# Optimization experiments

Hardware: AMD Instinct MI355X
Metric: run time of the kernel (lower is better)

The kernel has to match this reference:

```python
import jax, jax.numpy as jnp
import numpy as np

B, S, T, D, H, DF = 2, 2048, 2048, 1024, 16, 4096
DK = D // H
EPS = 1e-5


def _linear_params(key, d_in, d_out):
    kw, kb = jax.random.split(key)
    s = 1.0 / np.sqrt(d_in)
    W = jax.random.uniform(kw, (d_out, d_in), jnp.float32, -s, s)
    b = jax.random.uniform(kb, (d_out,), jnp.float32, -s, s)
    return W, b


def setup_inputs() -> dict:
    key = jax.random.key(0)
    ks = jax.random.split(key, 16)
    inp = {}
    inp['x'] = jax.random.normal(ks[0], (B, S, D), jnp.float32)
    inp['enc_out'] = jax.random.normal(ks[1], (B, T, D), jnp.float32)
    inp['src_mask'] = jnp.ones((B, 1, 1, T), jnp.int32)
    inp['tgt_mask'] = jnp.tril(jnp.ones((S, S), jnp.int32))[None, None, :, :]
    # self-attn params
    for i, nm in enumerate(['q1', 'k1', 'v1', 'o1']):
        W, b = _linear_params(ks[2 + i], D, D)
        inp['W' + nm], inp['b' + nm] = W, b
    # cross-attn params
    for i, nm in enumerate(['q2', 'k2', 'v2', 'o2']):
        W, b = _linear_params(ks[6 + i], D, D)
        inp['W' + nm], inp['b' + nm] = W, b
    # FFN
    inp['Wf1'], inp['bf1'] = _linear_params(ks[10], D, DF)
    inp['Wf2'], inp['bf2'] = _linear_params(ks[11], DF, D)
    # LayerNorms
    for i in (1, 2, 3):
        inp[f'g{i}'] = jnp.ones((D,), jnp.float32)
        inp[f'be{i}'] = jnp.zeros((D,), jnp.float32)
    return inp


def _lin(x, W, b):
    return x @ W.T + b


def _ln(x, g, b):
    mu = jnp.mean(x, -1, keepdims=True)
    var = jnp.mean(jnp.square(x - mu), -1, keepdims=True)
    return (x - mu) * jax.lax.rsqrt(var + EPS) * g + b


def _mha(q_in, k_in, v_in, Wq, bq, Wk, bk, Wv, bv, Wo, bo, mask):
    Bq = q_in.shape[0]
    q = _lin(q_in, Wq, bq).reshape(Bq, -1, H, DK).transpose(0, 2, 1, 3)
    k = _lin(k_in, Wk, bk).reshape(Bq, -1, H, DK).transpose(0, 2, 1, 3)
    v = _lin(v_in, Wv, bv).reshape(Bq, -1, H, DK).transpose(0, 2, 1, 3)
    scores = jnp.einsum('bhqd,bhkd->bhqk', q, k) / np.sqrt(DK)
    scores = jnp.where(mask == 0, -jnp.inf, scores)
    attn = jax.nn.softmax(scores, axis=-1)
    out = jnp.einsum('bhqk,bhkd->bhqd', attn, v)
    out = out.transpose(0, 2, 1, 3).reshape(Bq, -1, H * DK)
    return _lin(out, Wo, bo)


def reference(x, enc_out, src_mask, tgt_mask,
              Wq1, bq1, Wk1, bk1, Wv1, bv1, Wo1, bo1,
              Wq2, bq2, Wk2, bk2, Wv2, bv2, Wo2, bo2,
              Wf1, bf1, Wf2, bf2,
              g1, be1, g2, be2, g3, be3):
    out = _mha(x, x, x, Wq1, bq1, Wk1, bk1, Wv1, bv1, Wo1, bo1, tgt_mask)
    x = _ln(x + out, g1, be1)
    out = _mha(x, enc_out, enc_out, Wq2, bq2, Wk2, bk2, Wv2, bv2, Wo2, bo2, src_mask)
    x = _ln(x + out, g2, be2)
    ff = _lin(jax.nn.relu(_lin(x, Wf1, bf1)), Wf2, bf2)
    return _ln(x + ff, g3, be3)
```

## Files before the change

kernel.cpp:

```cpp
#include <hip/hip_runtime.h>


typedef __bf16 bf16_t;
typedef bf16_t  bf16x8 __attribute__((ext_vector_type(8)));
typedef float   f32x4  __attribute__((ext_vector_type(4)));
typedef unsigned short ushort_t;
typedef ushort_t u16x8 __attribute__((ext_vector_type(8)));
typedef ushort_t u16x4 __attribute__((ext_vector_type(4)));

__device__ __forceinline__ float b2f(ushort_t u) {
    union { unsigned u; float f; } x; x.u = ((unsigned)u) << 16; return x.f;
}
__device__ __forceinline__ ushort_t f2b(float f) {
    union { float f; unsigned u; } x; x.f = f;
    unsigned r = x.u + 0x7fffu + ((x.u >> 16) & 1u);
    return (ushort_t)(r >> 16);
}
__device__ __forceinline__ unsigned pk2(float lo, float hi) {
    union { float f; unsigned u; } a, b; a.f = lo; b.f = hi;
    return (b.u & 0xffff0000u) | (a.u >> 16);
}

#define GLL(gp, lp)                                                            \
    __builtin_amdgcn_global_load_lds(                                          \
        (const __attribute__((address_space(1))) void*)(gp),                   \
        (__attribute__((address_space(3))) void*)(lp), 16, 0, 0)

__global__ __launch_bounds__(256) void conv_all(
    const float* __restrict__ x,   const float* __restrict__ enc,
    const float* __restrict__ w0, const float* __restrict__ w1,
    const float* __restrict__ w2, const float* __restrict__ w3,
    const float* __restrict__ w4, const float* __restrict__ w5,
    const float* __restrict__ w6, const float* __restrict__ w7,
    const float* __restrict__ wf1, const float* __restrict__ wf2,
    ushort_t* __restrict__ Xb, ushort_t* __restrict__ Eb,
    ushort_t* __restrict__ Wb)
{
    const int b = blockIdx.x;
    const float* src;
    ushort_t* dst;
    size_t blk;
    if (b < 2048)      { src = x;   dst = Xb; blk = b; }
    else if (b < 4096) { src = enc; dst = Eb; blk = b - 2048; }
    else if (b < 8192) {
        const int i = (b - 4096) >> 9;
        src = (i < 4) ? (i < 2 ? (i == 0 ? w0 : w1) : (i == 2 ? w2 : w3))
                      : (i < 6 ? (i == 4 ? w4 : w5) : (i == 6 ? w6 : w7));
        dst = Wb + (size_t)i * 1048576;
        blk = (b - 4096) & 511;
    }
    else if (b < 10240) { src = wf1; dst = Wb + (size_t)8  * 1048576; blk = b - 8192; }
    else                { src = wf2; dst = Wb + (size_t)12 * 1048576; blk = b - 10240; }

    const size_t e = blk * 2048 + (size_t)threadIdx.x * 8;
    const float4 a = *(const float4*)(src + e);
    const float4 c = *(const float4*)(src + e + 4);
    uint4 r;
    r.x = pk2(a.x, a.y); r.y = pk2(a.z, a.w);
    r.z = pk2(c.x, c.y); r.w = pk2(c.z, c.w);
    *(uint4*)(dst + e) = r;
}

template <int EPI, int TM, bool RF32, bool FUSED, bool SPLITA, bool SPLITC,
          bool TRV>
__global__ __launch_bounds__(256) void gemm_bt(
    const ushort_t* __restrict__ A, const ushort_t* __restrict__ A2,
    const ushort_t* __restrict__ W,
    const float* __restrict__ b1, const float* __restrict__ b2,
    const float* __restrict__ b3,
    const void* __restrict__ Rv,
    ushort_t* __restrict__ C, ushort_t* __restrict__ C2,
    int M, int N, int K)
{
    constexpr int IM = TM / 32;
    __shared__ __align__(16) ushort_t At[TM * 32];
    __shared__ __align__(16) ushort_t Bt[128 * 32];

    const int tid  = threadIdx.x;
    const int lane = tid & 63, w = tid >> 6;
    const int g = lane >> 4, qi = lane & 15;

    const int nbn = gridDim.x, nbm = gridDim.y;
    const int lin = blockIdx.x + nbn * blockIdx.y;
    const int xcd = lin & 7, j = lin >> 3;
    const int bpx = nbm >> 3;
    const int bmb = xcd * bpx + (j & (bpx - 1));
    const int bnb = j / bpx;
    const int bm = bmb * TM, bn = bnb * 128;

    const int wm = (w >> 1) * (TM / 2), wn = (w & 1) * 64;

    const ushort_t* Ap = SPLITA ? ((bm < 2048) ? A : A2) : A;
    const int       am = SPLITA ? (bm & 2047) : bm;

    const int srow = lane >> 2;
    const int scol = (lane & 3) * 8;

    f32x4 acc[IM][4] = {};

    const int niter = K >> 5;
    for (int kt = 0; kt < niter; ++kt) {
        const int k0 = kt << 5;
        __syncthreads();
        if (TM == 128) {
#pragma unroll
            for (int c = 0; c < 2; ++c) {
                const int s = c * 4 + w;
                GLL(Ap + (size_t)(am + s * 16 + srow) * K + k0 + scol, At + s * 512);
            }
        } else {
            GLL(Ap + (size_t)(am + w * 16 + srow) * K + k0 + scol, At + w * 512);
        }
#pragma unroll
        for (int c = 0; c < 2; ++c) {
            const int s = c * 4 + w;
            GLL(W + (size_t)(bn + s * 16 + srow) * K + k0 + scol, Bt + s * 512);
        }
        __syncthreads();

        bf16x8 af[IM], bfr[4];
#pragma unroll
        for (int i = 0; i < IM; ++i)
            af[i] = *(const bf16x8*)(At + (wm + i * 16 + qi) * 32 + g * 8);
#pragma unroll
        for (int j2 = 0; j2 < 4; ++j2)
            bfr[j2] = *(const bf16x8*)(Bt + (wn + j2 * 16 + qi) * 32 + g * 8);
#pragma unroll
        for (int i = 0; i < IM; ++i)
#pragma unroll
            for (int j2 = 0; j2 < 4; ++j2)
                acc[i][j2] = __builtin_amdgcn_mfma_f32_16x16x32_bf16(
                    af[i], bfr[j2], acc[i][j2], 0, 0, 0);
    }

    const float* bp = FUSED ? (bn < 1024 ? b1 : (bn < 2048 ? b2 : b3)) : b1;
#pragma unroll
    for (int j2 = 0; j2 < 4; ++j2) {
        const int n = bn + wn + j2 * 16 + qi;
        const int nl = n & 1023;
        const float bv = bp[nl];
#pragma unroll
        for (int i = 0; i < IM; ++i) {
            if (EPI == 1 && TRV && bn >= N - 1024) {
                const int which = bn >> 10;
                const int h = nl >> 6, dk = nl & 63;
                const int m0 = bm + wm + i * 16 + g * 4;
                const int bb = m0 >> 11, s0 = m0 & 2047;
                u16x4 pv;
#pragma unroll
                for (int r = 0; r < 4; ++r) pv[r] = f2b(acc[i][j2][r] + bv);
                *(u16x4*)(C + (size_t)which * 4194304 +
                          (((size_t)((bb << 4) + h)) * 64 + dk) * 2048 + s0) = pv;
            } else {
#pragma unroll
                for (int r = 0; r < 4; ++r) {
                    const int m = bm + wm + i * 16 + g * 4 + r;
                    float v = acc[i][j2][r] + bv;
                    if (EPI == 2) {
                        v += RF32 ? ((const float*)Rv)[(size_t)m * N + n]
                                  : b2f(((const ushort_t*)Rv)[(size_t)m * N + n]);
                    }
                    if (EPI == 3) v = v > 0.f ? v : 0.f;
                    if (EPI == 1) {
                        const int which = FUSED ? (bn >> 10) : 0;
                        const int bb = m >> 11, s = m & 2047;
                        const int h = nl >> 6, dk = nl & 63;
                        const size_t dst = (size_t)which * 4194304 +
                            (((size_t)((bb << 4) + h)) * 2048 + s) * 64 + dk;
                        C[dst] = f2b(v);
                    } else {
                        ushort_t* Cp = SPLITC ? (m < 2048 ? C : C2) : C;
                        const int mr = SPLITC ? (m & 2047) : m;
                        Cp[(size_t)mr * N + n] = f2b(v);
                    }
                }
            }
        }
    }
}

template <bool CAUSAL>
__global__ __launch_bounds__(256) void flash_attn(
    const ushort_t* __restrict__ Q, const ushort_t* __restrict__ K,
    const ushort_t* __restrict__ V, ushort_t* __restrict__ O, int S)
{
    __shared__ __align__(16) ushort_t Kt[2][2048];
    __shared__ __align__(16) ushort_t Vt[2][2048];
    __shared__ __align__(16) ushort_t Pl[2048];

    const int tid = threadIdx.x, lane = tid & 63, w = tid >> 6;
    const int g = lane >> 4, qi = lane & 15;
    const int q2 = (qi >> 1) & 3;
    const int bh = blockIdx.x;
    const int y = blockIdx.y;
    const int qb = CAUSAL ? ((y & 8) ? ((y & 16) ? 55 - y : 23 - y) : y) : y;
    const size_t base = (size_t)bh * S * 64;
    const int q0 = qb << 6;
    const int qw = q0 + w * 16;

    constexpr float SC = 0.18033688011112042f;

    const int krow2 = ((w & 1) << 4) + (lane >> 2);
    const int kcol2 = ((w >> 1) << 5) + ((lane & 3) << 3);
    const ushort_t* Kp = K + base + (size_t)krow2 * 64 + kcol2;
    const ushort_t* Vp = V + base + (size_t)(w * 16 + (lane >> 2)) * 2048 +
                         ((lane & 3) << 3);

    bf16x8 qf0 = *(const bf16x8*)(Q + base + (size_t)(qw + qi) * 64 + g * 8);
    bf16x8 qf1 = *(const bf16x8*)(Q + base + (size_t)(qw + qi) * 64 + 32 + g * 8);
    asm volatile("" :: "v"(qf0), "v"(qf1));

    f32x4 oacc[4] = {};
    float lsum = 0.f;

    const int ntiles = CAUSAL ? ((q0 >> 5) + 2) : (S >> 5);

    GLL(Kp, &Kt[0][w * 512]);
    GLL(Vp, &Vt[0][w * 512]);
    asm volatile("s_waitcnt vmcnt(0)" ::: "memory");
    __builtin_amdgcn_s_barrier();
    __builtin_amdgcn_sched_barrier(0);

    for (int t = 0; t < ntiles; ++t) {
        const int cur = t & 1;
        const int k0 = t << 5;

        if (t + 1 < ntiles) {
            GLL(Kp + (size_t)(k0 + 32) * 64, &Kt[cur ^ 1][w * 512]);
            GLL(Vp + (k0 + 32), &Vt[cur ^ 1][w * 512]);
        }
        __builtin_amdgcn_sched_barrier(0);

        f32x4 st[2] = {};
        __builtin_amdgcn_s_setprio(1);
#pragma unroll
        for (int tt = 0; tt < 2; ++tt) {
            bf16x8 kf0 = *(const bf16x8*)(&Kt[cur][(tt * 16 + qi) * 32 + g * 8]);
            bf16x8 kf1 = *(const bf16x8*)(&Kt[cur][1024 + (tt * 16 + qi) * 32 + g * 8]);
            st[tt] = __builtin_amdgcn_mfma_f32_16x16x32_bf16(kf0, qf0, st[tt], 0, 0, 0);
            st[tt] = __builtin_amdgcn_mfma_f32_16x16x32_bf16(kf1, qf1, st[tt], 0, 0, 0);
        }
        __builtin_amdgcn_s_setprio(0);

        if (CAUSAL && (k0 + 31 > qw)) {
#pragma unroll
            for (int tt = 0; tt < 2; ++tt)
#pragma unroll
                for (int r = 0; r < 4; ++r)
                    if (k0 + tt * 16 + g * 4 + r > qw + qi) st[tt][r] = -1e30f;
        }

        float p[2][4];
#pragma unroll
        for (int tt = 0; tt < 2; ++tt)
#pragma unroll
            for (int r = 0; r < 4; ++r) {
                p[tt][r] = exp2f(st[tt][r] * SC);
                lsum += p[tt][r];
            }

        ushort_t* pb = Pl + w * 512;
#pragma unroll
        for (int tt = 0; tt < 2; ++tt) {
            unsigned lo, hi;
            asm("v_cvt_pk_bf16_f32 %0, %1, %2" : "=v"(lo) : "v"(p[tt][0]), "v"(p[tt][1]));
            asm("v_cvt_pk_bf16_f32 %0, %1, %2" : "=v"(hi) : "v"(p[tt][2]), "v"(p[tt][3]));
            const int swc = (tt * 2 + (g >> 1)) ^ q2;
            uint2 pw; pw.x = lo; pw.y = hi;
            *(uint2*)(pb + qi * 32 + swc * 8 + (g & 1) * 4) = pw;
        }
        asm volatile("s_waitcnt lgkmcnt(0)" ::: "memory");
        __builtin_amdgcn_sched_barrier(0);
        bf16x8 pf = *(const bf16x8*)(pb + qi * 32 + ((g ^ q2) << 3));

        __builtin_amdgcn_s_setprio(1);
#pragma unroll
        for (int dt = 0; dt < 4; ++dt) {
            bf16x8 vf = *(const bf16x8*)(&Vt[cur][(dt * 16 + qi) * 32 + g * 8]);
            oacc[dt] = __builtin_amdgcn_mfma_f32_16x16x32_bf16(pf, vf, oacc[dt], 0, 0, 0);
        }
        __builtin_amdgcn_s_setprio(0);

        asm volatile("s_waitcnt vmcnt(0)" ::: "memory");
        __builtin_amdgcn_s_barrier();
        __builtin_amdgcn_sched_barrier(0);
    }

    lsum += __shfl_xor(lsum, 16);
    lsum += __shfl_xor(lsum, 32);
    float lv[4];
#pragma unroll
    for (int r = 0; r < 4; ++r) lv[r] = 1.f / __shfl(lsum, g * 4 + r, 16);

    const int b = bh >> 4, h = bh & 15;
#pragma unroll
    for (int dt = 0; dt < 4; ++dt)
#pragma unroll
        for (int r = 0; r < 4; ++r) {
            const int row = b * S + qw + g * 4 + r;
            const int col = (h << 6) + dt * 16 + qi;
            O[(size_t)row * 1024 + col] = f2b(oacc[dt][r] * lv[r]);
        }
}

template <bool OUTF32>
__global__ __launch_bounds__(256) void ln_kernel(
    const ushort_t* __restrict__ X, const float* __restrict__ gam,
    const float* __restrict__ bet, void* __restrict__ Yv)
{
    const int row = blockIdx.x, tid = threadIdx.x;
    const int lane = tid & 63, w = tid >> 6;
    const size_t off = (size_t)row * 1024 + tid * 4;

    u16x4 xv = *(const u16x4*)(X + off);
    float f[4];
#pragma unroll
    for (int i = 0; i < 4; ++i) f[i] = b2f(xv[i]);

    float s = f[0] + f[1] + f[2] + f[3];
    float sq = f[0] * f[0] + f[1] * f[1] + f[2] * f[2] + f[3] * f[3];
#pragma unroll
    for (int o = 32; o; o >>= 1) {
        s  += __shfl_xor(s, o);
        sq += __shfl_xor(sq, o);
    }
    __shared__ float red[8];
    if (lane == 0) { red[w] = s; red[4 + w] = sq; }
    __syncthreads();
    s  = red[0] + red[1] + red[2] + red[3];
    sq = red[4] + red[5] + red[6] + red[7];

    const float mu = s * (1.f / 1024.f);
    const float var = sq * (1.f / 1024.f) - mu * mu;
    const float rs = rsqrtf(var + 1e-5f);

    const float4 gv = *(const float4*)(gam + tid * 4);
    const float4 bv = *(const float4*)(bet + tid * 4);
    float y0 = (f[0] - mu) * rs * gv.x + bv.x;
    float y1 = (f[1] - mu) * rs * gv.y + bv.y;
    float y2 = (f[2] - mu) * rs * gv.z + bv.z;
    float y3 = (f[3] - mu) * rs * gv.w + bv.w;

    if (OUTF32) {
        float4 yv; yv.x = y0; yv.y = y1; yv.z = y2; yv.w = y3;
        *(float4*)((float*)Yv + off) = yv;
    } else {
        u16x4 yv;
        yv[0] = f2b(y0); yv[1] = f2b(y1); yv[2] = f2b(y2); yv[3] = f2b(y3);
        *(u16x4*)((ushort_t*)Yv + off) = yv;
    }
}

extern "C" void kernel_launch(void* const* d_in, const int* in_sizes, int n_in,
                              void* d_out, int out_size, void* d_ws, size_t ws_size,
                              hipStream_t stream)
{
    const float* x   = (const float*)d_in[0];
    const float* enc = (const float*)d_in[1];
    const float* Wq1 = (const float*)d_in[4];
    const float* bq1 = (const float*)d_in[5];
    const float* Wk1 = (const float*)d_in[6];
    const float* bk1 = (const float*)d_in[7];
    const float* Wv1 = (const float*)d_in[8];
    const float* bv1 = (const float*)d_in[9];
    const float* Wo1 = (const float*)d_in[10];
    const float* bo1 = (const float*)d_in[11];
    const float* Wq2 = (const float*)d_in[12];
    const float* bq2 = (const float*)d_in[13];
    const float* Wk2 = (const float*)d_in[14];
    const float* bk2 = (const float*)d_in[15];
    const float* Wv2 = (const float*)d_in[16];
    const float* bv2 = (const float*)d_in[17];
    const float* Wo2 = (const float*)d_in[18];
    const float* bo2 = (const float*)d_in[19];
    const float* Wf1 = (const float*)d_in[20];
    const float* bf1 = (const float*)d_in[21];
    const float* Wf2 = (const float*)d_in[22];
    const float* bf2 = (const float*)d_in[23];
    const float* gm1 = (const float*)d_in[24];
    const float* be1 = (const float*)d_in[25];
    const float* gm2 = (const float*)d_in[26];
    const float* be2 = (const float*)d_in[27];
    const float* gm3 = (const float*)d_in[28];
    const float* be3 = (const float*)d_in[29];

    float*    out = (float*)d_out;
    ushort_t* ws  = (ushort_t*)d_ws;
    ushort_t* F2  = (ushort_t*)d_out;

    const size_t E = (size_t)4096 * 1024;
    ushort_t* P0 = ws;
    ushort_t* P1 = ws + 1 * E;
    ushort_t* P2 = ws + 2 * E;
    ushort_t* P3 = ws + 3 * E;
    ushort_t* P4 = ws + 4 * E;
    ushort_t* Wb = ws + 5 * E;

    const size_t M1 = 1048576;
    ushort_t* Wb_qkv1 = Wb;
    ushort_t* Wb_o1   = Wb + 3 * M1;
    ushort_t* Wb_q2   = Wb + 4 * M1;
    ushort_t* Wb_kv2  = Wb + 5 * M1;
    ushort_t* Wb_o2   = Wb + 7 * M1;
    ushort_t* Wb_f1   = Wb + 8 * M1;
    ushort_t* Wb_f2   = Wb + 12 * M1;

    const dim3 blk(256);
    const dim3 gA(32, 32);

    conv_all<<<12288, blk, 0, stream>>>(x, enc, Wq1, Wk1, Wv1, Wo1, Wq2, Wk2,
                                        Wv2, Wo2, Wf1, Wf2, P3, P4, Wb);

    gemm_bt<1, 128, false, true, false, false, true><<<dim3(24, 32), blk, 0, stream>>>(
        P3, nullptr, Wb_qkv1, bq1, bk1, bv1, nullptr, P0, nullptr, 4096, 3072, 1024);
    flash_attn<true><<<gA, blk, 0, stream>>>(P0, P1, P2, P3, 2048);
    gemm_bt<2, 64, true, false, false, false, false><<<dim3(8, 64), blk, 0, stream>>>(
        P3, nullptr, Wb_o1, bo1, bo1, bo1, x, P0, nullptr, 4096, 1024, 1024);
    ln_kernel<false><<<4096, blk, 0, stream>>>(P0, gm1, be1, P1);

    gemm_bt<1, 64, false, false, false, false, false><<<dim3(8, 64), blk, 0, stream>>>(
        P1, nullptr, Wb_q2, bq2, bq2, bq2, nullptr, P0, nullptr, 4096, 1024, 1024);
    gemm_bt<1, 128, false, true, false, false, true><<<dim3(16, 32), blk, 0, stream>>>(
        P4, nullptr, Wb_kv2, bk2, bv2, bv2, nullptr, P2, nullptr, 4096, 2048, 1024);
    flash_attn<false><<<gA, blk, 0, stream>>>(P0, P2, P3, P4, 2048);
    gemm_bt<2, 64, false, false, false, false, false><<<dim3(8, 64), blk, 0, stream>>>(
        P4, nullptr, Wb_o2, bo2, bo2, bo2, P1, P0, nullptr, 4096, 1024, 1024);
    ln_kernel<false><<<4096, blk, 0, stream>>>(P0, gm2, be2, P2);

    gemm_bt<3, 128, false, false, false, true, false><<<dim3(32, 32), blk, 0, stream>>>(
        P2, nullptr, Wb_f1, bf1, bf1, bf1, nullptr, P0, F2, 4096, 4096, 1024);
    gemm_bt<2, 64, false, false, true, false, false><<<dim3(8, 64), blk, 0, stream>>>(
        P0, F2, Wb_f2, bf2, bf2, bf2, P2, P3, nullptr, 4096, 1024, 4096);
    ln_kernel<true><<<4096, blk, 0, stream>>>(P3, gm3, be3, out);
}
```

Baseline: 593.8 us.

## Triple-buffer flash attention K/V tiles and fold softmax scale into Q projection

Flash attention now keeps three K/V tile buffers in LDS and prefetches two tiles ahead, waiting only on the older loads (vmcnt(2)) so global loads overlap more compute. The softmax scale (1/sqrt(dk)·log2e) is folded into the Q-projection GEMM epilogue, which removes a multiply per score. It also uses the hardware exp2 builtin instead of exp2f. The cost is more LDS per block, which may lower occupancy, and rounding Q to bf16 after scaling changes precision slightly.

```diff
diff --git a/kernel.cpp b/kernel.cpp
--- a/kernel.cpp
+++ b/kernel.cpp
@@ -20,6 +20,12 @@
     union { float f; unsigned u; } a, b; a.f = lo; b.f = hi;
     return (b.u & 0xffff0000u) | (a.u >> 16);
 }
+
+#if __has_builtin(__builtin_amdgcn_exp2f)
+#define EXP2(x) __builtin_amdgcn_exp2f(x)
+#else
+#define EXP2(x) exp2f(x)
+#endif
 
 #define GLL(gp, lp)                                                            \
     __builtin_amdgcn_global_load_lds(                                          \
@@ -62,7 +68,7 @@
 }
 
 template <int EPI, int TM, bool RF32, bool FUSED, bool SPLITA, bool SPLITC,
-          bool TRV>
+          bool TRV, bool QSC>
 __global__ __launch_bounds__(256) void gemm_bt(
     const ushort_t* __restrict__ A, const ushort_t* __restrict__ A2,
     const ushort_t* __restrict__ W,
@@ -163,6 +169,8 @@
                     if (EPI == 3) v = v > 0.f ? v : 0.f;
                     if (EPI == 1) {
                         const int which = FUSED ? (bn >> 10) : 0;
+                        if (QSC && which == 0)
+                            v *= 0.18033688011112042f;
                         const int bb = m >> 11, s = m & 2047;
                         const int h = nl >> 6, dk = nl & 63;
                         const size_t dst = (size_t)which * 4194304 +
@@ -184,8 +192,8 @@
     const ushort_t* __restrict__ Q, const ushort_t* __restrict__ K,
     const ushort_t* __restrict__ V, ushort_t* __restrict__ O, int S)
 {
-    __shared__ __align__(16) ushort_t Kt[2][2048];
-    __shared__ __align__(16) ushort_t Vt[2][2048];
+    __shared__ __align__(16) ushort_t Kt[3][2048];
+    __shared__ __align__(16) ushort_t Vt[3][2048];
     __shared__ __align__(16) ushort_t Pl[2048];
 
     const int tid = threadIdx.x, lane = tid & 63, w = tid >> 6;
@@ -198,8 +206,6 @@
     const int q0 = qb << 6;
     const int qw = q0 + w * 16;
 
-    constexpr float SC = 0.18033688011112042f;
-
     const int krow2 = ((w & 1) << 4) + (lane >> 2);
     const int kcol2 = ((w >> 1) << 5) + ((lane & 3) << 3);
     const ushort_t* Kp = K + base + (size_t)krow2 * 64 + kcol2;
@@ -217,17 +223,21 @@
 
     GLL(Kp, &Kt[0][w * 512]);
     GLL(Vp, &Vt[0][w * 512]);
-    asm volatile("s_waitcnt vmcnt(0)" ::: "memory");
+    GLL(Kp + (size_t)32 * 64, &Kt[1][w * 512]);
+    GLL(Vp + 32, &Vt[1][w * 512]);
+    asm volatile("s_waitcnt vmcnt(2)" ::: "memory");
     __builtin_amdgcn_s_barrier();
     __builtin_amdgcn_sched_barrier(0);
 
+    int c0 = 0;
     for (int t = 0; t < ntiles; ++t) {
-        const int cur = t & 1;
-        const int k0 = t << 5;
-
-        if (t + 1 < ntiles) {
-            GLL(Kp + (size_t)(k0 + 32) * 64, &Kt[cur ^ 1][w * 512]);
-            GLL(Vp + (k0 + 32), &Vt[cur ^ 1][w * 512]);
+        const bool pre = (t + 2 < ntiles);
+
+        if (pre) {
+            const int kn = (t + 2) << 5;
+            int cn = c0 + 2; if (cn >= 3) cn -= 3;
+            GLL(Kp + (size_t)kn * 64, &Kt[cn][w * 512]);
+            GLL(Vp + kn, &Vt[cn][w * 512]);
         }
         __builtin_amdgcn_sched_barrier(0);
 
@@ -235,13 +245,14 @@
         __builtin_amdgcn_s_setprio(1);
 #pragma unroll
         for (int tt = 0; tt < 2; ++tt) {
-            bf16x8 kf0 = *(const bf16x8*)(&Kt[cur][(tt * 16 + qi) * 32 + g * 8]);
-            bf16x8 kf1 = *(const bf16x8*)(&Kt[cur][1024 + (tt * 16 + qi) * 32 + g * 8]);
+            bf16x8 kf0 = *(const bf16x8*)(&Kt[c0][(tt * 16 + qi) * 32 + g * 8]);
+            bf16x8 kf1 = *(const bf16x8*)(&Kt[c0][1024 + (tt * 16 + qi) * 32 + g * 8]);
             st[tt] = __builtin_amdgcn_mfma_f32_16x16x32_bf16(kf0, qf0, st[tt], 0, 0, 0);
             st[tt] = __builtin_amdgcn_mfma_f32_16x16x32_bf16(kf1, qf1, st[tt], 0, 0, 0);
         }
         __builtin_amdgcn_s_setprio(0);
 
+        const int k0 = t << 5;
         if (CAUSAL && (k0 + 31 > qw)) {
 #pragma unroll
             for (int tt = 0; tt < 2; ++tt)
@@ -255,7 +266,7 @@
         for (int tt = 0; tt < 2; ++tt)
 #pragma unroll
             for (int r = 0; r < 4; ++r) {
-                p[tt][r] = exp2f(st[tt][r] * SC);
+                p[tt][r] = EXP2(st[tt][r]);
                 lsum += p[tt][r];
             }
 
@@ -276,14 +287,19 @@
         __builtin_amdgcn_s_setprio(1);
 #pragma unroll
         for (int dt = 0; dt < 4; ++dt) {
-            bf16x8 vf = *(const bf16x8*)(&Vt[cur][(dt * 16 + qi) * 32 + g * 8]);
+            bf16x8 vf = *(const bf16x8*)(&Vt[c0][(dt * 16 + qi) * 32 + g * 8]);
             oacc[dt] = __builtin_amdgcn_mfma_f32_16x16x32_bf16(pf, vf, oacc[dt], 0, 0, 0);
         }
         __builtin_amdgcn_s_setprio(0);
 
-        asm volatile("s_waitcnt vmcnt(0)" ::: "memory");
+        if (pre) {
+            asm volatile("s_waitcnt vmcnt(2)" ::: "memory");
+        } else {
+            asm volatile("s_waitcnt vmcnt(0)" ::: "memory");
+        }
         __builtin_amdgcn_s_barrier();
         __builtin_amdgcn_sched_barrier(0);
+        if (++c0 == 3) c0 = 0;
     }
 
     lsum += __shfl_xor(lsum, 16);
@@ -411,25 +427,25 @@
     conv_all<<<12288, blk, 0, stream>>>(x, enc, Wq1, Wk1, Wv1, Wo1, Wq2, Wk2,
                                         Wv2, Wo2, Wf1, Wf2, P3, P4, Wb);
 
-    gemm_bt<1, 128, false, true, false, false, true><<<dim3(24, 32), blk, 0, stream>>>(
+    gemm_bt<1, 128, false, true, false, false, true, true><<<dim3(24, 32), blk, 0, stream>>>(
         P3, nullptr, Wb_qkv1, bq1, bk1, bv1, nullptr, P0, nullptr, 4096, 3072, 1024);
     flash_attn<true><<<gA, blk, 0, stream>>>(P0, P1, P2, P3, 2048);
-    gemm_bt<2, 64, true, false, false, false, false><<<dim3(8, 64), blk, 0, stream>>>(
+    gemm_bt<2, 64, true, false, false, false, false, false><<<dim3(8, 64), blk, 0, stream>>>(
         P3, nullptr, Wb_o1, bo1, bo1, bo1, x, P0, nullptr, 4096, 1024, 1024);
     ln_kernel<false><<<4096, blk, 0, stream>>>(P0, gm1, be1, P1);
 
-    gemm_bt<1, 64, false, false, false, false, false><<<dim3(8, 64), blk, 0, stream>>>(
+    gemm_bt<1, 64, false, false, false, false, false, true><<<dim3(8, 64), blk, 0, stream>>>(
         P1, nullptr, Wb_q2, bq2, bq2, bq2, nullptr, P0, nullptr, 4096, 1024, 1024);
-    gemm_bt<1, 128, false, true, false, false, true><<<dim3(16, 32), blk, 0, stream>>>(
+    gemm_bt<1, 128, false, true, false, false, true, false><<<dim3(16, 32), blk, 0, stream>>>(
         P4, nullptr, Wb_kv2, bk2, bv2, bv2, nullptr, P2, nullptr, 4096, 2048, 1024);
     flash_attn<false><<<gA, blk, 0, stream>>>(P0, P2, P3, P4, 2048);
-    gemm_bt<2, 64, false, false, false, false, false><<<dim3(8, 64), blk, 0, stream>>>(
+    gemm_bt<2, 64, false, false, false, false, false, false><<<dim3(8, 64), blk, 0, stream>>>(
         P4, nullptr, Wb_o2, bo2, bo2, bo2, P1, P0, nullptr, 4096, 1024, 1024);
     ln_kernel<false><<<4096, blk, 0, stream>>>(P0, gm2, be2, P2);
 
-    gemm_bt<3, 128, false, false, false, true, false><<<dim3(32, 32), blk, 0, stream>>>(
+    gemm_bt<3, 128, false, false, false, true, false, false><<<dim3(32, 32), blk, 0, stream>>>(
         P2, nullptr, Wb_f1, bf1, bf1, bf1, nullptr, P0, F2, 4096, 4096, 1024);
-    gemm_bt<2, 64, false, false, true, false, false><<<dim3(8, 64), blk, 0, stream>>>(
+    gemm_bt<2, 64, false, false, true, false, false, false><<<dim3(8, 64), blk, 0, stream>>>(
         P0, F2, Wb_f2, bf2, bf2, bf2, P2, P3, nullptr, 4096, 1024, 4096);
     ln_kernel<true><<<4096, blk, 0, stream>>>(P3, gm3, be3, out);
 }
```

Result: faster. 577.4 us (-2.8%).
